# Performance work log

Hardware: AMD Instinct MI355X
Metric: run time of the kernel (lower is better)

## Reference

```python
import jax, jax.numpy as jnp
import numpy as np

D_MODEL = 512
NUM_HEADS = 8
HEAD_DIM = D_MODEL // NUM_HEADS
SEQ_LEN = 4096


def setup_inputs() -> dict:
    key = jax.random.key(0)
    ks = jax.random.split(key, 6)
    s = 1.0 / np.sqrt(D_MODEL)
    return {
        "x": jax.random.normal(ks[0], (SEQ_LEN, D_MODEL), jnp.float32),
        "wq": jax.random.normal(ks[1], (D_MODEL, D_MODEL), jnp.float32) * s,
        "bq": jnp.zeros((D_MODEL,), jnp.float32),
        "wk": jax.random.normal(ks[2], (D_MODEL, D_MODEL), jnp.float32) * s,
        "bk": jnp.zeros((D_MODEL,), jnp.float32),
        "wv": jax.random.normal(ks[3], (D_MODEL, D_MODEL), jnp.float32) * s,
        "bv": jnp.zeros((D_MODEL,), jnp.float32),
        "wo": jax.random.normal(ks[4], (D_MODEL, D_MODEL), jnp.float32) * s,
        "bo": jnp.zeros((D_MODEL,), jnp.float32),
    }


def reference(x, wq, bq, wk, bk, wv, bv, wo, bo):
    seq_len, d_model = x.shape
    # projections (nn.Linear: x @ W^T + b)
    q = x @ wq.T + bq
    k = x @ wk.T + bk
    v = x @ wv.T + bv
    # [seq, H, hd] -> [H, seq, hd]
    q = q.reshape(seq_len, NUM_HEADS, HEAD_DIM).transpose(1, 0, 2)
    k = k.reshape(seq_len, NUM_HEADS, HEAD_DIM).transpose(1, 0, 2)
    v = v.reshape(seq_len, NUM_HEADS, HEAD_DIM).transpose(1, 0, 2)
    scale = 1.0 / np.sqrt(HEAD_DIM).astype(np.float32)
    scores = jnp.einsum('hqd,hkd->hqk', q, k) * scale  # [H, S, S]
    causal = jnp.tril(jnp.ones((seq_len, seq_len), bool))  # True = keep
    scores = jnp.where(causal[None, :, :], scores, jnp.float32(-jnp.inf))
    attn = jax.nn.softmax(scores, axis=-1)
    out = jnp.einsum('hqk,hkd->hqd', attn, v)  # [H, S, hd]
    out = out.transpose(1, 0, 2).reshape(seq_len, d_model)
    return out @ wo.T + bo
```

## Files before the change

### kernel.cpp

```cpp
#include <hip/hip_runtime.h>

#define S_LEN 4096
#define DMODEL 512
#define NHEADS 8
#define HDIM 64

typedef unsigned short u16;
typedef __bf16 bf16x8 __attribute__((ext_vector_type(8)));
typedef float f32x4 __attribute__((ext_vector_type(4)));

__device__ __forceinline__ u16 f2b(float f) {
  union { float f; unsigned u; } v;
  v.f = f;
  return (u16)((v.u + 0x7FFFu + ((v.u >> 16) & 1u)) >> 16);
}

typedef const unsigned int __attribute__((address_space(1)))* gas1_u32p;
typedef unsigned int __attribute__((address_space(3)))* las3_u32p;
__device__ __forceinline__ void gload16(const void* g, void* l) {
  __builtin_amdgcn_global_load_lds((gas1_u32p)g, (las3_u32p)l, 16, 0, 0);
}

__global__ __launch_bounds__(256)
void to_bf16_all(const float* __restrict__ x,  const float* __restrict__ wq,
                 const float* __restrict__ wk, const float* __restrict__ wv,
                 const float* __restrict__ wo,
                 u16* __restrict__ x16,  u16* __restrict__ wq16,
                 u16* __restrict__ wk16, u16* __restrict__ wv16,
                 u16* __restrict__ wo16) {
  const float* s; u16* d; int n;
  switch (blockIdx.z) {
    case 0:  s = x;  d = x16;  n = S_LEN * DMODEL;  break;
    case 1:  s = wq; d = wq16; n = DMODEL * DMODEL; break;
    case 2:  s = wk; d = wk16; n = DMODEL * DMODEL; break;
    case 3:  s = wv; d = wv16; n = DMODEL * DMODEL; break;
    default: s = wo; d = wo16; n = DMODEL * DMODEL; break;
  }
  int i = (int)(blockIdx.x * 256 + threadIdx.x) * 4;
  if (i >= n) return;
  const float4 v = *(const float4*)(s + i);
  ushort4 o;
  o.x = f2b(v.x); o.y = f2b(v.y); o.z = f2b(v.z); o.w = f2b(v.w);
  *(ushort4*)(d + i) = o;
}

template <int OUTMODE>
__device__ __forceinline__ void gemm128_body(
    const u16* __restrict__ A16, const u16* __restrict__ W16,
    const float* __restrict__ bias, void* __restrict__ Cout,
    int bm, int bn) {
  __shared__ __align__(16) u16 As[128 * 32];
  __shared__ __align__(16) u16 Ws[128 * 32];

  const int tid  = threadIdx.x;
  const int wid  = tid >> 6;
  const int lane = tid & 63;
  const int lg   = lane >> 4;
  const int lr   = lane & 15;
  const int wr   = wid >> 1;
  const int wc   = wid & 1;

  f32x4 acc[4][4] = {};

  for (int k0 = 0; k0 < DMODEL; k0 += 32) {
    __syncthreads();
    {
      const int i0 = tid, i1 = tid + 256;
      gload16(A16 + (size_t)(bm + (i0 >> 2)) * DMODEL + k0 + (i0 & 3) * 8, &As[i0 * 8]);
      gload16(A16 + (size_t)(bm + (i1 >> 2)) * DMODEL + k0 + (i1 & 3) * 8, &As[i1 * 8]);
      gload16(W16 + (size_t)(bn + (i0 >> 2)) * DMODEL + k0 + (i0 & 3) * 8, &Ws[i0 * 8]);
      gload16(W16 + (size_t)(bn + (i1 >> 2)) * DMODEL + k0 + (i1 & 3) * 8, &Ws[i1 * 8]);
    }
    __syncthreads();

    bf16x8 af[4], bf[4];
    #pragma unroll
    for (int mi = 0; mi < 4; ++mi)
      af[mi] = *(const bf16x8*)&As[(wr * 64 + mi * 16 + lr) * 32 + lg * 8];
    #pragma unroll
    for (int ni = 0; ni < 4; ++ni)
      bf[ni] = *(const bf16x8*)&Ws[(wc * 64 + ni * 16 + lr) * 32 + lg * 8];

    __builtin_amdgcn_s_setprio(1);
    #pragma unroll
    for (int mi = 0; mi < 4; ++mi)
      #pragma unroll
      for (int ni = 0; ni < 4; ++ni)
        acc[mi][ni] = __builtin_amdgcn_mfma_f32_16x16x32_bf16(
            af[mi], bf[ni], acc[mi][ni], 0, 0, 0);
    __builtin_amdgcn_s_setprio(0);
  }

  #pragma unroll
  for (int mi = 0; mi < 4; ++mi)
    #pragma unroll
    for (int ni = 0; ni < 4; ++ni) {
      const int col = bn + wc * 64 + ni * 16 + lr;
      const float bval = bias[col];
      const int row0 = bm + wr * 64 + mi * 16 + lg * 4;
      if (OUTMODE == 2) {
        ushort4 o4;
        o4.x = f2b(acc[mi][ni][0] + bval);
        o4.y = f2b(acc[mi][ni][1] + bval);
        o4.z = f2b(acc[mi][ni][2] + bval);
        o4.w = f2b(acc[mi][ni][3] + bval);
        *(ushort4*)((u16*)Cout + (size_t)col * S_LEN + row0) = o4;
      } else {
        #pragma unroll
        for (int r = 0; r < 4; ++r) {
          const float val = acc[mi][ni][r] + bval;
          if (OUTMODE == 1)
            ((u16*)Cout)[(size_t)(row0 + r) * DMODEL + col] = f2b(val);
          else
            ((float*)Cout)[(size_t)(row0 + r) * DMODEL + col] = val;
        }
      }
    }
}

__global__ __launch_bounds__(256)
void gemm_qkv(const u16* __restrict__ x16,
              const u16* __restrict__ wq16, const u16* __restrict__ wk16,
              const u16* __restrict__ wv16,
              const float* __restrict__ bq, const float* __restrict__ bk,
              const float* __restrict__ bvv,
              u16* __restrict__ Qm, u16* __restrict__ Km, u16* __restrict__ Vt) {
  const int bm = blockIdx.y * 128, bn = blockIdx.x * 128;
  if (blockIdx.z == 0)
    gemm128_body<1>(x16, wq16, bq, Qm, bm, bn);
  else if (blockIdx.z == 1)
    gemm128_body<1>(x16, wk16, bk, Km, bm, bn);
  else
    gemm128_body<2>(x16, wv16, bvv, Vt, bm, bn);
}

__global__ __launch_bounds__(256)
void gemm_o(const u16* __restrict__ Am, const u16* __restrict__ wo16,
            const float* __restrict__ bo, float* __restrict__ out) {
  gemm128_body<0>(Am, wo16, bo, out, blockIdx.y * 128, blockIdx.x * 128);
}

__global__ __launch_bounds__(256)
void flash_attn_mfma(const u16* __restrict__ Qg, const u16* __restrict__ Kg,
                     const u16* __restrict__ Vt, u16* __restrict__ Og) {
  const int id   = (int)blockIdx.x;
  const int j    = id & 255;
  const int head = j & 7;
  const int qi   = j >> 3;
  const int qb   = (id < 256) ? (63 - qi) : qi;
  const int q0   = qb * 64;
  const int tid  = threadIdx.x;
  const int wid  = tid >> 6;
  const int lane = tid & 63;
  const int lg   = lane >> 4;
  const int lr   = lane & 15;

  __shared__ __align__(16) u16    Ks[2][2][64][32];
  __shared__ __align__(16) u16    Vs[2][2][64][32];
  __shared__ __align__(16) __bf16 Ps[64][72];

  bf16x8 qa[2];
  #pragma unroll
  for (int ks = 0; ks < 2; ++ks)
    qa[ks] = *(const bf16x8*)(Qg + (size_t)(q0 + wid * 16 + lr) * DMODEL +
                              head * HDIM + ks * 32 + lg * 8);

  const int sr = tid >> 2;
  const int sc = (tid & 3) * 8;
  const u16* Kbase = Kg + head * HDIM;
  const u16* Vbase = Vt + (size_t)head * HDIM * S_LEN;

#define STAGE(k0_, buf_) {                                                    \
    gload16(Kbase + (size_t)((k0_) + sr) * DMODEL + sc,      &Ks[buf_][0][sr][sc]); \
    gload16(Kbase + (size_t)((k0_) + sr) * DMODEL + 32 + sc, &Ks[buf_][1][sr][sc]); \
    gload16(Vbase + (size_t)sr * S_LEN + (k0_) + sc,         &Vs[buf_][0][sr][sc]); \
    gload16(Vbase + (size_t)sr * S_LEN + (k0_) + 32 + sc,    &Vs[buf_][1][sr][sc]); \
  }

  float l_sum[4] = {0.0f, 0.0f, 0.0f, 0.0f};
  f32x4 oacc[4] = {};
  const float SC = 0.125f * 1.44269504f;

  STAGE(0, 0)
  __syncthreads();

  for (int kb = 0; kb <= qb; ++kb) {
    const int cur = kb & 1;
    const int k0  = kb * 64;

    if (kb < qb) STAGE(k0 + 64, cur ^ 1)

    f32x4 s[4] = {};
    __builtin_amdgcn_s_setprio(1);
    #pragma unroll
    for (int c = 0; c < 4; ++c)
      #pragma unroll
      for (int ks = 0; ks < 2; ++ks) {
        const bf16x8 kf = *(const bf16x8*)&Ks[cur][ks][c * 16 + lr][lg * 8];
        s[c] = __builtin_amdgcn_mfma_f32_16x16x32_bf16(qa[ks], kf, s[c], 0, 0, 0);
      }
    __builtin_amdgcn_s_setprio(0);

    const bool diag = (kb == qb);
    #pragma unroll
    for (int r = 0; r < 4; ++r) {
      const int rowg = q0 + wid * 16 + lg * 4 + r;
      #pragma unroll
      for (int c = 0; c < 4; ++c) {
        const int colg = k0 + c * 16 + lr;
        const float p = (!diag || colg <= rowg) ? exp2f(s[c][r] * SC) : 0.0f;
        Ps[wid * 16 + lg * 4 + r][c * 16 + lr] = (__bf16)p;
        l_sum[r] += p;
      }
    }

    bf16x8 pa[2];
    #pragma unroll
    for (int ks = 0; ks < 2; ++ks)
      pa[ks] = *(const bf16x8*)&Ps[wid * 16 + lr][ks * 32 + lg * 8];
    __builtin_amdgcn_s_setprio(1);
    #pragma unroll
    for (int c2 = 0; c2 < 4; ++c2)
      #pragma unroll
      for (int ks = 0; ks < 2; ++ks) {
        const bf16x8 vf = *(const bf16x8*)&Vs[cur][ks][c2 * 16 + lr][lg * 8];
        oacc[c2] = __builtin_amdgcn_mfma_f32_16x16x32_bf16(pa[ks], vf, oacc[c2], 0, 0, 0);
      }
    __builtin_amdgcn_s_setprio(0);

    if (kb < qb) __syncthreads();
  }

  #pragma unroll
  for (int r = 0; r < 4; ++r) {
    float l = l_sum[r];
    #pragma unroll
    for (int off = 1; off < 16; off <<= 1)
      l += __shfl_xor(l, off, 64);
    const float inv = 1.0f / l;
    const int rowg = q0 + wid * 16 + lg * 4 + r;
    #pragma unroll
    for (int c2 = 0; c2 < 4; ++c2)
      Og[(size_t)rowg * DMODEL + head * HDIM + c2 * 16 + lr] =
          f2b(oacc[c2][r] * inv);
  }
#undef STAGE
}

extern "C" void kernel_launch(void* const* d_in, const int* in_sizes, int n_in,
                              void* d_out, int out_size, void* d_ws, size_t ws_size,
                              hipStream_t stream) {
  const float* x  = (const float*)d_in[0];
  const float* wq = (const float*)d_in[1];
  const float* bq = (const float*)d_in[2];
  const float* wk = (const float*)d_in[3];
  const float* bk = (const float*)d_in[4];
  const float* wv = (const float*)d_in[5];
  const float* bv = (const float*)d_in[6];
  const float* wo = (const float*)d_in[7];
  const float* bo = (const float*)d_in[8];
  float* out = (float*)d_out;

  const size_t MAT = (size_t)S_LEN * DMODEL;
  const size_t WMAT = (size_t)DMODEL * DMODEL;
  u16* x16  = (u16*)d_ws;
  u16* wq16 = x16  + MAT;
  u16* wk16 = wq16 + WMAT;
  u16* wv16 = wk16 + WMAT;
  u16* wo16 = wv16 + WMAT;
  u16* Qm   = wo16 + WMAT;
  u16* Km   = Qm + MAT;
  u16* Vt   = Km + MAT;
  u16* Am   = Vt + MAT;

  to_bf16_all<<<dim3(2048, 1, 5), 256, 0, stream>>>(
      x, wq, wk, wv, wo, x16, wq16, wk16, wv16, wo16);

  gemm_qkv<<<dim3(DMODEL / 128, S_LEN / 128, 3), 256, 0, stream>>>(
      x16, wq16, wk16, wv16, bq, bk, bv, Qm, Km, Vt);

  flash_attn_mfma<<<512, 256, 0, stream>>>(Qm, Km, Vt, Am);

  gemm_o<<<dim3(DMODEL / 128, S_LEN / 128), 256, 0, stream>>>(Am, wo16, bo, out);
}
```

Before: 185.6 us.

## Split causal attention over two key ranges with atomic merge, fuse QKV GEMM

Each query block's key range is split into two halves run by separate workgroups. This doubles the grid and balances causal work. Partial unnormalized outputs and row sums are accumulated with fp32 atomics into a zeroed buffer, then a new merge kernel normalizes them to bf16. The change also gives the three projections a single concatenated-weight GEMM launch, swaps direct global-to-LDS loads for register-staged K/V loads, and XOR-swizzles the P tile in LDS to reduce bank conflicts. In exchange it adds a memset, atomic traffic on a large fp32 buffer, an extra kernel, and extra barriers per tile.

```diff
diff --git a/kernel.cpp b/kernel.cpp
--- a/kernel.cpp
+++ b/kernel.cpp
@@ -8,6 +8,7 @@
 typedef unsigned short u16;
 typedef __bf16 bf16x8 __attribute__((ext_vector_type(8)));
 typedef float f32x4 __attribute__((ext_vector_type(4)));
+typedef unsigned short ushort8v __attribute__((ext_vector_type(8)));
 
 __device__ __forceinline__ u16 f2b(float f) {
   union { float f; unsigned u; } v;
@@ -44,23 +45,18 @@
   *(ushort4*)(d + i) = o;
 }
 
-template <int OUTMODE>
-__device__ __forceinline__ void gemm128_body(
+__device__ __forceinline__ void gemm_core(
     const u16* __restrict__ A16, const u16* __restrict__ W16,
-    const float* __restrict__ bias, void* __restrict__ Cout,
-    int bm, int bn) {
+    int bm, int bn, f32x4 (&acc)[4][4]) {
   __shared__ __align__(16) u16 As[128 * 32];
   __shared__ __align__(16) u16 Ws[128 * 32];
-
-  const int tid  = threadIdx.x;
+  const int tid = threadIdx.x;
+  const int lane = tid & 63;
   const int wid  = tid >> 6;
-  const int lane = tid & 63;
   const int lg   = lane >> 4;
   const int lr   = lane & 15;
   const int wr   = wid >> 1;
   const int wc   = wid & 1;
-
-  f32x4 acc[4][4] = {};
 
   for (int k0 = 0; k0 < DMODEL; k0 += 32) {
     __syncthreads();
@@ -90,64 +86,97 @@
             af[mi], bf[ni], acc[mi][ni], 0, 0, 0);
     __builtin_amdgcn_s_setprio(0);
   }
+}
+
+__global__ __launch_bounds__(256)
+void gemm_qkv_fused(const u16* __restrict__ x16, const u16* __restrict__ Wcat,
+                    const float* __restrict__ bq, const float* __restrict__ bk,
+                    const float* __restrict__ bvv,
+                    u16* __restrict__ Qm, u16* __restrict__ Km,
+                    u16* __restrict__ Vt) {
+  const int bm = blockIdx.y * 128;
+  const int bng = blockIdx.x * 128;
+  const int proj = bng >> 9;
+  f32x4 acc[4][4] = {};
+  gemm_core(x16, Wcat, bm, bng, acc);
+
+  const int tid = threadIdx.x;
+  const int lane = tid & 63;
+  const int wid  = tid >> 6;
+  const int lg   = lane >> 4;
+  const int lr   = lane & 15;
+  const int wr   = wid >> 1;
+  const int wc   = wid & 1;
+  const float* bp = (proj == 0) ? bq : (proj == 1) ? bk : bvv;
+  u16* outQK = (proj == 0) ? Qm : Km;
 
   #pragma unroll
   for (int mi = 0; mi < 4; ++mi)
     #pragma unroll
     for (int ni = 0; ni < 4; ++ni) {
-      const int col = bn + wc * 64 + ni * 16 + lr;
-      const float bval = bias[col];
+      const int colg = bng + wc * 64 + ni * 16 + lr;
+      const int col  = colg & 511;
+      const float bval = bp[col];
       const int row0 = bm + wr * 64 + mi * 16 + lg * 4;
-      if (OUTMODE == 2) {
+      if (proj == 2) {
         ushort4 o4;
         o4.x = f2b(acc[mi][ni][0] + bval);
         o4.y = f2b(acc[mi][ni][1] + bval);
         o4.z = f2b(acc[mi][ni][2] + bval);
         o4.w = f2b(acc[mi][ni][3] + bval);
-        *(ushort4*)((u16*)Cout + (size_t)col * S_LEN + row0) = o4;
+        *(ushort4*)(Vt + (size_t)col * S_LEN + row0) = o4;
       } else {
         #pragma unroll
-        for (int r = 0; r < 4; ++r) {
-          const float val = acc[mi][ni][r] + bval;
-          if (OUTMODE == 1)
-            ((u16*)Cout)[(size_t)(row0 + r) * DMODEL + col] = f2b(val);
-          else
-            ((float*)Cout)[(size_t)(row0 + r) * DMODEL + col] = val;
-        }
+        for (int r = 0; r < 4; ++r)
+          outQK[(size_t)(row0 + r) * DMODEL + col] = f2b(acc[mi][ni][r] + bval);
       }
     }
-}
-
-__global__ __launch_bounds__(256)
-void gemm_qkv(const u16* __restrict__ x16,
-              const u16* __restrict__ wq16, const u16* __restrict__ wk16,
-              const u16* __restrict__ wv16,
-              const float* __restrict__ bq, const float* __restrict__ bk,
-              const float* __restrict__ bvv,
-              u16* __restrict__ Qm, u16* __restrict__ Km, u16* __restrict__ Vt) {
-  const int bm = blockIdx.y * 128, bn = blockIdx.x * 128;
-  if (blockIdx.z == 0)
-    gemm128_body<1>(x16, wq16, bq, Qm, bm, bn);
-  else if (blockIdx.z == 1)
-    gemm128_body<1>(x16, wk16, bk, Km, bm, bn);
-  else
-    gemm128_body<2>(x16, wv16, bvv, Vt, bm, bn);
 }
 
 __global__ __launch_bounds__(256)
 void gemm_o(const u16* __restrict__ Am, const u16* __restrict__ wo16,
             const float* __restrict__ bo, float* __restrict__ out) {
-  gemm128_body<0>(Am, wo16, bo, out, blockIdx.y * 128, blockIdx.x * 128);
-}
-
-__global__ __launch_bounds__(256)
-void flash_attn_mfma(const u16* __restrict__ Qg, const u16* __restrict__ Kg,
-                     const u16* __restrict__ Vt, u16* __restrict__ Og) {
+  const int bm = blockIdx.y * 128, bn = blockIdx.x * 128;
+  f32x4 acc[4][4] = {};
+  gemm_core(Am, wo16, bm, bn, acc);
+  const int tid = threadIdx.x;
+  const int lane = tid & 63;
+  const int wid  = tid >> 6;
+  const int lg   = lane >> 4;
+  const int lr   = lane & 15;
+  const int wr   = wid >> 1;
+  const int wc   = wid & 1;
+  #pragma unroll
+  for (int mi = 0; mi < 4; ++mi)
+    #pragma unroll
+    for (int ni = 0; ni < 4; ++ni) {
+      const int col = bn + wc * 64 + ni * 16 + lr;
+      const float bval = bo[col];
+      const int row0 = bm + wr * 64 + mi * 16 + lg * 4;
+      #pragma unroll
+      for (int r = 0; r < 4; ++r)
+        out[(size_t)(row0 + r) * DMODEL + col] = acc[mi][ni][r] + bval;
+    }
+}
+
+__global__ __launch_bounds__(256)
+void flash_attn_partial(const u16* __restrict__ Qg, const u16* __restrict__ Kg,
+                        const u16* __restrict__ Vt, float* __restrict__ Oacc,
+                        float* __restrict__ lacc) {
   const int id   = (int)blockIdx.x;
-  const int j    = id & 255;
-  const int head = j & 7;
-  const int qi   = j >> 3;
-  const int qb   = (id < 256) ? (63 - qi) : qi;
+  const int g    = id & 255;
+  const int k4   = id >> 8;
+  const int head = g & 7;
+  const int q1   = g >> 3;
+  const int qb   = (k4 < 2) ? q1 : 63 - q1;
+  const int half = k4 & 1;
+  const int n    = qb + 1;
+  const int mid  = (n + 1) >> 1;
+  const int kb0  = half ? mid : 0;
+  const int kb1  = half ? n : mid;
+  const int nt   = kb1 - kb0;
+  if (nt <= 0) return;
+
   const int q0   = qb * 64;
   const int tid  = threadIdx.x;
   const int wid  = tid >> 6;
@@ -157,7 +186,7 @@
 
   __shared__ __align__(16) u16    Ks[2][2][64][32];
   __shared__ __align__(16) u16    Vs[2][2][64][32];
-  __shared__ __align__(16) __bf16 Ps[64][72];
+  __shared__ __align__(16) __bf16 Ps[64 * 64];
 
   bf16x8 qa[2];
   #pragma unroll
@@ -165,30 +194,39 @@
     qa[ks] = *(const bf16x8*)(Qg + (size_t)(q0 + wid * 16 + lr) * DMODEL +
                               head * HDIM + ks * 32 + lg * 8);
 
-  const int sr = tid >> 2;
-  const int sc = (tid & 3) * 8;
+  const int sr  = tid >> 2;
+  const int sc8 = (tid & 3) * 8;
   const u16* Kbase = Kg + head * HDIM;
   const u16* Vbase = Vt + (size_t)head * HDIM * S_LEN;
-
-#define STAGE(k0_, buf_) {                                                    \
-    gload16(Kbase + (size_t)((k0_) + sr) * DMODEL + sc,      &Ks[buf_][0][sr][sc]); \
-    gload16(Kbase + (size_t)((k0_) + sr) * DMODEL + 32 + sc, &Ks[buf_][1][sr][sc]); \
-    gload16(Vbase + (size_t)sr * S_LEN + (k0_) + sc,         &Vs[buf_][0][sr][sc]); \
-    gload16(Vbase + (size_t)sr * S_LEN + (k0_) + 32 + sc,    &Vs[buf_][1][sr][sc]); \
+  ushort8v kreg[2], vreg[2];
+
+#define LOAD_TILE(k0_) {                                                      \
+    kreg[0] = *(const ushort8v*)(Kbase + (size_t)((k0_) + sr) * DMODEL + sc8);      \
+    kreg[1] = *(const ushort8v*)(Kbase + (size_t)((k0_) + sr) * DMODEL + 32 + sc8); \
+    vreg[0] = *(const ushort8v*)(Vbase + (size_t)sr * S_LEN + (k0_) + sc8);         \
+    vreg[1] = *(const ushort8v*)(Vbase + (size_t)sr * S_LEN + (k0_) + 32 + sc8);    \
+  }
+#define STORE_TILE(buf_) {                                                    \
+    *(ushort8v*)&Ks[buf_][0][sr][sc8] = kreg[0];                              \
+    *(ushort8v*)&Ks[buf_][1][sr][sc8] = kreg[1];                              \
+    *(ushort8v*)&Vs[buf_][0][sr][sc8] = vreg[0];                              \
+    *(ushort8v*)&Vs[buf_][1][sr][sc8] = vreg[1];                              \
   }
 
   float l_sum[4] = {0.0f, 0.0f, 0.0f, 0.0f};
   f32x4 oacc[4] = {};
   const float SC = 0.125f * 1.44269504f;
 
-  STAGE(0, 0)
+  LOAD_TILE(kb0 * 64)
+  STORE_TILE(0)
   __syncthreads();
 
-  for (int kb = 0; kb <= qb; ++kb) {
-    const int cur = kb & 1;
+  for (int t = 0; t < nt; ++t) {
+    const int kb  = kb0 + t;
+    const int cur = t & 1;
     const int k0  = kb * 64;
 
-    if (kb < qb) STAGE(k0 + 64, cur ^ 1)
+    if (t + 1 < nt) LOAD_TILE(k0 + 64)
 
     f32x4 s[4] = {};
     __builtin_amdgcn_s_setprio(1);
@@ -204,20 +242,26 @@
     const bool diag = (kb == qb);
     #pragma unroll
     for (int r = 0; r < 4; ++r) {
-      const int rowg = q0 + wid * 16 + lg * 4 + r;
+      const int row  = wid * 16 + lg * 4 + r;
+      const int rowg = q0 + row;
+      const int X    = (row & 7) << 3;
       #pragma unroll
       for (int c = 0; c < 4; ++c) {
         const int colg = k0 + c * 16 + lr;
         const float p = (!diag || colg <= rowg) ? exp2f(s[c][r] * SC) : 0.0f;
-        Ps[wid * 16 + lg * 4 + r][c * 16 + lr] = (__bf16)p;
+        Ps[row * 64 + ((c * 16 + lr) ^ X)] = (__bf16)p;
         l_sum[r] += p;
       }
     }
 
     bf16x8 pa[2];
-    #pragma unroll
-    for (int ks = 0; ks < 2; ++ks)
-      pa[ks] = *(const bf16x8*)&Ps[wid * 16 + lr][ks * 32 + lg * 8];
+    {
+      const int row2 = wid * 16 + lr;
+      const int X2   = (lr & 7) << 3;
+      #pragma unroll
+      for (int ks = 0; ks < 2; ++ks)
+        pa[ks] = *(const bf16x8*)&Ps[row2 * 64 + ((ks * 32 + lg * 8) ^ X2)];
+    }
     __builtin_amdgcn_s_setprio(1);
     #pragma unroll
     for (int c2 = 0; c2 < 4; ++c2)
@@ -228,7 +272,11 @@
       }
     __builtin_amdgcn_s_setprio(0);
 
-    if (kb < qb) __syncthreads();
+    if (t + 1 < nt) {
+      __syncthreads();
+      STORE_TILE(1 - cur)
+      __syncthreads();
+    }
   }
 
   #pragma unroll
@@ -237,14 +285,30 @@
     #pragma unroll
     for (int off = 1; off < 16; off <<= 1)
       l += __shfl_xor(l, off, 64);
-    const float inv = 1.0f / l;
     const int rowg = q0 + wid * 16 + lg * 4 + r;
+    if (lr == 0) atomicAdd(&lacc[head * S_LEN + rowg], l);
     #pragma unroll
     for (int c2 = 0; c2 < 4; ++c2)
-      Og[(size_t)rowg * DMODEL + head * HDIM + c2 * 16 + lr] =
-          f2b(oacc[c2][r] * inv);
-  }
-#undef STAGE
+      atomicAdd(&Oacc[(size_t)rowg * DMODEL + head * HDIM + c2 * 16 + lr],
+                oacc[c2][r]);
+  }
+#undef LOAD_TILE
+#undef STORE_TILE
+}
+
+__global__ __launch_bounds__(256)
+void merge_norm(const float* __restrict__ Oacc, const float* __restrict__ lacc,
+                u16* __restrict__ Am) {
+  const int e4  = (int)(blockIdx.x * 256 + threadIdx.x);
+  const int row = e4 >> 7;
+  const int c4  = (e4 & 127) * 4;
+  const int head = c4 >> 6;
+  const float inv = 1.0f / lacc[head * S_LEN + row];
+  const float4 v = *(const float4*)&Oacc[(size_t)row * DMODEL + c4];
+  ushort4 o;
+  o.x = f2b(v.x * inv); o.y = f2b(v.y * inv);
+  o.z = f2b(v.z * inv); o.w = f2b(v.w * inv);
+  *(ushort4*)(Am + (size_t)row * DMODEL + c4) = o;
 }
 
 extern "C" void kernel_launch(void* const* d_in, const int* in_sizes, int n_in,
@@ -261,7 +325,7 @@
   const float* bo = (const float*)d_in[8];
   float* out = (float*)d_out;
 
-  const size_t MAT = (size_t)S_LEN * DMODEL;
+  const size_t MAT  = (size_t)S_LEN * DMODEL;
   const size_t WMAT = (size_t)DMODEL * DMODEL;
   u16* x16  = (u16*)d_ws;
   u16* wq16 = x16  + MAT;
@@ -272,14 +336,20 @@
   u16* Km   = Qm + MAT;
   u16* Vt   = Km + MAT;
   u16* Am   = Vt + MAT;
+  float* Oacc = (float*)(Am + MAT);
+  float* lacc = Oacc + MAT;
+
+  hipMemsetAsync(Oacc, 0, (MAT + (size_t)NHEADS * S_LEN) * sizeof(float), stream);
 
   to_bf16_all<<<dim3(2048, 1, 5), 256, 0, stream>>>(
       x, wq, wk, wv, wo, x16, wq16, wk16, wv16, wo16);
 
-  gemm_qkv<<<dim3(DMODEL / 128, S_LEN / 128, 3), 256, 0, stream>>>(
-      x16, wq16, wk16, wv16, bq, bk, bv, Qm, Km, Vt);
-
-  flash_attn_mfma<<<512, 256, 0, stream>>>(Qm, Km, Vt, Am);
-
-  gemm_o<<<dim3(DMODEL / 128, S_LEN / 128), 256, 0, stream>>>(Am, wo16, bo, out);
-}
+  gemm_qkv_fused<<<dim3(12, 32), 256, 0, stream>>>(
+      x16, wq16, bq, bk, bv, Qm, Km, Vt);
+
+  flash_attn_partial<<<1024, 256, 0, stream>>>(Qm, Km, Vt, Oacc, lacc);
+
+  merge_norm<<<2048, 256, 0, stream>>>(Oacc, lacc, Am);
+
+  gemm_o<<<dim3(4, 32), 256, 0, stream>>>(Am, wo16, bo, out);
+}
```

After: 178.5 us. 3.8% less time.
